# Performance work log

Hardware: AMD Instinct MI355X
Metric: run time of the kernel (lower is better)

## Reference

```python
import jax, jax.numpy as jnp
import numpy as np


def setup_inputs() -> dict:
    key = jax.random.key(0)
    ks = jax.random.split(key, 8)
    N, E = 100000, 3200000
    IN, H, OUT = 256, 128, 64
    x = jax.random.normal(ks[0], (N, IN), dtype=jnp.float32)
    src = jax.random.randint(ks[1], (E,), 0, N, dtype=jnp.int64)
    dst = jax.random.randint(ks[2], (E,), 0, N, dtype=jnp.int64)
    # Glorot-ish scaled weights
    W1_self = jax.random.normal(ks[3], (IN, H), dtype=jnp.float32) / np.sqrt(IN)
    W1_neigh = jax.random.normal(ks[4], (IN, H), dtype=jnp.float32) / np.sqrt(IN)
    b1 = jnp.zeros((H,), dtype=jnp.float32)
    W2_self = jax.random.normal(ks[5], (H, OUT), dtype=jnp.float32) / np.sqrt(H)
    W2_neigh = jax.random.normal(ks[6], (H, OUT), dtype=jnp.float32) / np.sqrt(H)
    b2 = jnp.zeros((OUT,), dtype=jnp.float32)
    return {"x": x, "src": src, "dst": dst,
            "W1_self": W1_self, "W1_neigh": W1_neigh, "b1": b1,
            "W2_self": W2_self, "W2_neigh": W2_neigh, "b2": b2}


def _sage_mean(h, src, dst, W_self, W_neigh, b, deg_inv):
    # mean aggregation over in-neighbors (edges src -> dst)
    N = h.shape[0]
    agg = jax.ops.segment_sum(h[src], dst, num_segments=N)  # [N, F]
    h_neigh = agg * deg_inv[:, None]
    return h @ W_self + h_neigh @ W_neigh + b


def reference(x, src, dst, W1_self, W1_neigh, b1, W2_self, W2_neigh, b2):
    N = x.shape[0]
    deg = jax.ops.segment_sum(jnp.ones_like(dst, dtype=x.dtype), dst, num_segments=N)
    deg_inv = 1.0 / jnp.maximum(deg, 1.0)  # DGL clamps in-degree to >= 1
    h = _sage_mean(x, src, dst, W1_self, W1_neigh, b1, deg_inv)
    h = jax.nn.relu(h)
    h = _sage_mean(h, src, dst, W2_self, W2_neigh, b2, deg_inv)
    return h
```

## Files before the change

### kernel.cpp

```cpp
#include <hip/hip_runtime.h>
#include <hip/hip_bf16.h>


typedef unsigned int uint32;
typedef __attribute__((ext_vector_type(8))) short short8;
typedef __attribute__((ext_vector_type(4))) float f32x4;

#define NBMAX 1024
#define EPB   8192

#if defined(__has_builtin)
#if __has_builtin(__builtin_amdgcn_cvt_pk_f32_fp8) && __has_builtin(__builtin_amdgcn_cvt_pk_fp8_f32)
#define FP8_HW 1
#endif
#endif
#ifndef FP8_HW
#define FP8_HW 0
#endif

__device__ __forceinline__ unsigned short f2bf(float f) {
    unsigned u = __float_as_uint(f);
    u += 0x7fffu + ((u >> 16) & 1u);
    return (unsigned short)(u >> 16);
}
__device__ __forceinline__ uint32 pack2bf(float lo, float hi) {
    return (uint32)f2bf(lo) | ((uint32)f2bf(hi) << 16);
}
__device__ __forceinline__ float bf_lo(uint32 v) { return __uint_as_float(v << 16); }
__device__ __forceinline__ float bf_hi(uint32 v) { return __uint_as_float(v & 0xFFFF0000u); }

__device__ __forceinline__ unsigned char enc8(float v) {
#if FP8_HW
    return (unsigned char)(__builtin_amdgcn_cvt_pk_fp8_f32(v, v, 0, false) & 0xFF);
#else
    float g = v * 0x1p-120f;
    uint32 b = __float_as_uint(g);
    uint32 s = (b >> 24) & 0x80u;
    b &= 0x7fffffffu;
    b += 0x7ffffu + ((b >> 20) & 1u);
    int t = (int)(b >> 20) - 960;
    t = t < 0 ? 0 : (t > 126 ? 126 : t);
    return (unsigned char)(s | (uint32)t);
#endif
}
#if !FP8_HW
__device__ __forceinline__ float dec1(uint32 b) {
    uint32 bits = ((b & 0x80u) << 24) | ((b & 0x7fu) << 20);
    return __uint_as_float(bits) * 0x1p+120f;
}
#endif
__device__ __forceinline__ void dec_u32(uint32 u, float& f0, float& f1, float& f2, float& f3) {
#if FP8_HW
    auto lo = __builtin_amdgcn_cvt_pk_f32_fp8(u, false);
    auto hi = __builtin_amdgcn_cvt_pk_f32_fp8(u, true);
    f0 = lo[0]; f1 = lo[1]; f2 = hi[0]; f3 = hi[1];
#else
    f0 = dec1(u & 0xffu); f1 = dec1((u >> 8) & 0xffu);
    f2 = dec1((u >> 16) & 0xffu); f3 = dec1(u >> 24);
#endif
}

__global__ __launch_bounds__(256) void k_bucket_count(const int* __restrict__ dst, int E,
                                                      int* __restrict__ bcnt) {
    __shared__ int hist[NBMAX];
    for (int i = threadIdx.x; i < NBMAX; i += 256) hist[i] = 0;
    __syncthreads();
    int base = blockIdx.x * EPB;
    #pragma unroll 4
    for (int i = 0; i < EPB / 256; ++i) {
        int e = base + i * 256 + threadIdx.x;
        if (e < E) atomicAdd(&hist[dst[e] >> 7], 1);
    }
    __syncthreads();
    for (int i = threadIdx.x; i < NBMAX; i += 256) {
        int h = hist[i];
        if (h) atomicAdd(&bcnt[i], h);
    }
}

__global__ __launch_bounds__(1024) void k_bucket_scan(const int* __restrict__ bcnt, int NB,
                                                      int* __restrict__ boffs, int* __restrict__ gfill,
                                                      int E) {
    __shared__ int sd[1024];
    int tid = threadIdx.x;
    int v = (tid < NB) ? bcnt[tid] : 0;
    sd[tid] = v;
    __syncthreads();
    for (int off = 1; off < 1024; off <<= 1) {
        int t = (tid >= off) ? sd[tid - off] : 0;
        __syncthreads();
        sd[tid] += t;
        __syncthreads();
    }
    int excl = sd[tid] - v;
    if (tid < NB) { boffs[tid] = excl; gfill[tid] = excl; }
    if (tid == 0) boffs[NB] = E;
}

__global__ __launch_bounds__(256) void k_bucket_scatter(const int* __restrict__ src,
                                                        const int* __restrict__ dst, int E,
                                                        int* __restrict__ gfill,
                                                        uint32* __restrict__ pairs) {
    __shared__ int hist[NBMAX];
    __shared__ int basea[NBMAX];
    for (int i = threadIdx.x; i < NBMAX; i += 256) hist[i] = 0;
    __syncthreads();
    int base = blockIdx.x * EPB;
    #pragma unroll 4
    for (int i = 0; i < EPB / 256; ++i) {
        int e = base + i * 256 + threadIdx.x;
        if (e < E) atomicAdd(&hist[dst[e] >> 7], 1);
    }
    __syncthreads();
    for (int i = threadIdx.x; i < NBMAX; i += 256) {
        int h = hist[i];
        basea[i] = h ? atomicAdd(&gfill[i], h) : 0;
        hist[i] = 0;
    }
    __syncthreads();
    #pragma unroll 4
    for (int i = 0; i < EPB / 256; ++i) {
        int e = base + i * 256 + threadIdx.x;
        if (e < E) {
            int d = dst[e];
            int b = d >> 7;
            int pos = basea[b] + atomicAdd(&hist[b], 1);
            pairs[pos] = ((uint32)src[e] << 7) | (uint32)(d & 127);
        }
    }
}

__global__ __launch_bounds__(256) void k_bucket_sort(const uint32* __restrict__ pairs,
                                                     const int* __restrict__ boffs,
                                                     int N, int E,
                                                     int* __restrict__ row_start,
                                                     float* __restrict__ deg_inv,
                                                     int* __restrict__ src_sorted) {
    __shared__ int cnt[128];
    __shared__ int sc[128];
    __shared__ int fill[128];
    int b = blockIdx.x, tid = threadIdx.x;
    int s0 = boffs[b], s1 = boffs[b + 1];
    if (tid < 128) cnt[tid] = 0;
    __syncthreads();
    for (int e = s0 + tid; e < s1; e += 256)
        atomicAdd(&cnt[pairs[e] & 127], 1);
    __syncthreads();
    if (tid < 128) sc[tid] = cnt[tid];
    __syncthreads();
    for (int off = 1; off < 128; off <<= 1) {
        int v = 0;
        if (tid < 128 && tid >= off) v = sc[tid - off];
        __syncthreads();
        if (tid < 128) sc[tid] += v;
        __syncthreads();
    }
    if (tid < 128) {
        int excl = sc[tid] - cnt[tid];
        int node = b * 128 + tid;
        if (node < N) {
            row_start[node] = s0 + excl;
            int d = cnt[tid];
            deg_inv[node] = 1.0f / (float)(d > 1 ? d : 1);
        }
        fill[tid] = s0 + excl;
    }
    if (b == 0 && tid == 0) row_start[N] = E;
    __syncthreads();
    for (int e = s0 + tid; e < s1; e += 256) {
        uint32 p = pairs[e];
        int pos = atomicAdd(&fill[p & 127], 1);
        src_sorted[pos] = (int)(p >> 7);
    }
}

__global__ __launch_bounds__(256) void k_cast_x(const float* __restrict__ x, uint32* __restrict__ xb,
                                                long n8, long total8) {
    long t = (long)blockIdx.x * blockDim.x + threadIdx.x;
    if (t >= total8) return;
    uint4 o = make_uint4(0u, 0u, 0u, 0u);
    if (t < n8) {
        const float4* p = reinterpret_cast<const float4*>(x) + t * 2;
        float4 a = p[0], b = p[1];
        o.x = pack2bf(a.x, a.y); o.y = pack2bf(a.z, a.w);
        o.z = pack2bf(b.x, b.y); o.w = pack2bf(b.z, b.w);
    }
    reinterpret_cast<uint4*>(xb)[t] = o;
}

__global__ __launch_bounds__(256) void k_wt(const float* __restrict__ Ws, const float* __restrict__ Wn,
                                            int K, int logK, int halfC, unsigned short* __restrict__ Wt) {
    int t = blockIdx.x * blockDim.x + threadIdx.x;
    int total = 2 * halfC * K;
    if (t >= total) return;
    int c = t >> logK, k = t & (K - 1);
    float v = (c < halfC) ? Ws[(size_t)k * halfC + c] : Wn[(size_t)k * halfC + (c - halfC)];
    Wt[t] = f2bf(v);
}

template<int K, int NF, bool YSPLIT>
__global__ __launch_bounds__(512) void gemm_rs(const unsigned short* __restrict__ A, int nstrip,
                                               const unsigned short* __restrict__ Wt,
                                               unsigned short* __restrict__ S16,
                                               unsigned char* __restrict__ N8) {
    constexpr int KS = K / 32;
    __shared__ unsigned short Bs[NF * KS * 512];
    const int tid = threadIdx.x;
    const int wave = tid >> 6, lane = tid & 63;
    const int l15 = lane & 15, l4 = lane >> 4;

    const unsigned short* Wtblk = Wt + (YSPLIT ? (size_t)blockIdx.y * 128 * K : 0);
    const bool out8 = YSPLIT && (blockIdx.y == 1);

    for (int i = tid; i < NF * KS * 64; i += 512) {
        int f = i >> 6, l = i & 63;
        int s = f / NF, n = f - s * NF;
        int col = n * 16 + (l & 15);
        int k = s * 32 + (l >> 4) * 8;
        uint4 v = *reinterpret_cast<const uint4*>(&Wtblk[(size_t)col * K + k]);
        *reinterpret_cast<uint4*>(&Bs[(size_t)i * 8]) = v;
    }
    __syncthreads();

    const unsigned short* Bl = Bs + (size_t)lane * 8;
    const int stride = gridDim.x;
    int g = blockIdx.x;
    if (g >= nstrip) return;

    uint4 uA[KS], uB[KS];

    auto loadA = [&](int gg, uint4* u) {
        int arow = gg * 128 + wave * 16 + l15;
        const unsigned short* Ar = A + (size_t)arow * K + l4 * 8;
        #pragma unroll
        for (int s = 0; s < KS; ++s)
            u[s] = *reinterpret_cast<const uint4*>(Ar + s * 32);
    };

    auto compute = [&](int gc, uint4* u) {
        f32x4 acc[NF] = {};
        #pragma unroll
        for (int s = 0; s < KS; ++s) {
            union { uint4 q; short8 v; } cv;
            cv.q = u[s];
            short8 af = cv.v;
            #pragma unroll
            for (int n = 0; n < NF; ++n) {
                short8 bf = *reinterpret_cast<const short8*>(Bl + (size_t)(s * NF + n) * 512);
                acc[n] = __builtin_amdgcn_mfma_f32_16x16x32_bf16(af, bf, acc[n], 0, 0, 0);
            }
        }
        const int rbase = gc * 128 + wave * 16;
        #pragma unroll
        for (int n = 0; n < NF; ++n) {
            #pragma unroll
            for (int r = 0; r < 4; ++r) {
                int rw = rbase + l4 * 4 + r;
                if constexpr (YSPLIT) {
                    int col = n * 16 + l15;
                    if (out8) N8[(size_t)rw * 128 + col] = enc8(acc[n][r]);
                    else      S16[(size_t)rw * 128 + col] = f2bf(acc[n][r]);
                } else {
                    if (n < 4) S16[(size_t)rw * 64 + n * 16 + l15] = f2bf(acc[n][r]);
                    else       N8[(size_t)rw * 64 + (n - 4) * 16 + l15] = enc8(acc[n][r]);
                }
            }
        }
    };

    loadA(g, uA);
    while (true) {
        int gn = g + stride;
        if (gn < nstrip) loadA(gn, uB);
        compute(g, uA);
        if (gn >= nstrip) break;
        g = gn;
        gn = g + stride;
        if (gn < nstrip) loadA(gn, uA);
        compute(g, uB);
        if (gn >= nstrip) break;
        g = gn;
    }
}

__global__ __launch_bounds__(256) void k_agg1(const uint2* __restrict__ t1n, const uint4* __restrict__ t1s,
                                              const int* __restrict__ rs, const int* __restrict__ ss,
                                              const float* __restrict__ dinv, const float* __restrict__ b1,
                                              uint4* __restrict__ h, int N) {
    int wid  = (blockIdx.x * blockDim.x + threadIdx.x) >> 6;
    int lane = threadIdx.x & 63;
    if (wid >= N) return;
    int e0 = rs[wid], e1 = rs[wid + 1];
    const int q = lane >> 4, c = lane & 15;
    float a0 = 0, a1 = 0, a2 = 0, a3 = 0, a4 = 0, a5 = 0, a6 = 0, a7 = 0;
    float f0, f1, f2, f3;
    int e = e0;
    for (; e + 16 <= e1; e += 16) {
        int s0 = ss[e + q];
        int s1 = ss[e + 4 + q];
        int s2 = ss[e + 8 + q];
        int s3 = ss[e + 12 + q];
        uint2 v0 = t1n[(size_t)s0 * 16 + c];
        uint2 v1 = t1n[(size_t)s1 * 16 + c];
        uint2 v2 = t1n[(size_t)s2 * 16 + c];
        uint2 v3 = t1n[(size_t)s3 * 16 + c];
        dec_u32(v0.x, f0, f1, f2, f3); a0 += f0; a1 += f1; a2 += f2; a3 += f3;
        dec_u32(v0.y, f0, f1, f2, f3); a4 += f0; a5 += f1; a6 += f2; a7 += f3;
        dec_u32(v1.x, f0, f1, f2, f3); a0 += f0; a1 += f1; a2 += f2; a3 += f3;
        dec_u32(v1.y, f0, f1, f2, f3); a4 += f0; a5 += f1; a6 += f2; a7 += f3;
        dec_u32(v2.x, f0, f1, f2, f3); a0 += f0; a1 += f1; a2 += f2; a3 += f3;
        dec_u32(v2.y, f0, f1, f2, f3); a4 += f0; a5 += f1; a6 += f2; a7 += f3;
        dec_u32(v3.x, f0, f1, f2, f3); a0 += f0; a1 += f1; a2 += f2; a3 += f3;
        dec_u32(v3.y, f0, f1, f2, f3); a4 += f0; a5 += f1; a6 += f2; a7 += f3;
    }
    for (; e < e1; e += 4) {
        if (e + q < e1) {
            int s = ss[e + q];
            uint2 v = t1n[(size_t)s * 16 + c];
            dec_u32(v.x, f0, f1, f2, f3); a0 += f0; a1 += f1; a2 += f2; a3 += f3;
            dec_u32(v.y, f0, f1, f2, f3); a4 += f0; a5 += f1; a6 += f2; a7 += f3;
        }
    }
    a0 += __shfl_xor(a0, 16); a1 += __shfl_xor(a1, 16); a2 += __shfl_xor(a2, 16); a3 += __shfl_xor(a3, 16);
    a4 += __shfl_xor(a4, 16); a5 += __shfl_xor(a5, 16); a6 += __shfl_xor(a6, 16); a7 += __shfl_xor(a7, 16);
    a0 += __shfl_xor(a0, 32); a1 += __shfl_xor(a1, 32); a2 += __shfl_xor(a2, 32); a3 += __shfl_xor(a3, 32);
    a4 += __shfl_xor(a4, 32); a5 += __shfl_xor(a5, 32); a6 += __shfl_xor(a6, 32); a7 += __shfl_xor(a7, 32);
    if (lane < 16) {
        float di = dinv[wid];
        uint4 sv = t1s[(size_t)wid * 16 + c];
        float4 bA = *reinterpret_cast<const float4*>(&b1[c * 8]);
        float4 bB = *reinterpret_cast<const float4*>(&b1[c * 8 + 4]);
        float h0 = fmaxf(fmaf(a0, di, bf_lo(sv.x)) + bA.x, 0.f);
        float h1 = fmaxf(fmaf(a1, di, bf_hi(sv.x)) + bA.y, 0.f);
        float h2 = fmaxf(fmaf(a2, di, bf_lo(sv.y)) + bA.z, 0.f);
        float h3 = fmaxf(fmaf(a3, di, bf_hi(sv.y)) + bA.w, 0.f);
        float h4 = fmaxf(fmaf(a4, di, bf_lo(sv.z)) + bB.x, 0.f);
        float h5 = fmaxf(fmaf(a5, di, bf_hi(sv.z)) + bB.y, 0.f);
        float h6 = fmaxf(fmaf(a6, di, bf_lo(sv.w)) + bB.z, 0.f);
        float h7 = fmaxf(fmaf(a7, di, bf_hi(sv.w)) + bB.w, 0.f);
        uint4 o;
        o.x = pack2bf(h0, h1); o.y = pack2bf(h2, h3);
        o.z = pack2bf(h4, h5); o.w = pack2bf(h6, h7);
        h[(size_t)wid * 16 + c] = o;
    }
}

__global__ __launch_bounds__(256) void k_agg2(const uint2* __restrict__ t2n, const uint4* __restrict__ t2s,
                                              const int* __restrict__ rs, const int* __restrict__ ss,
                                              const float* __restrict__ dinv, const float* __restrict__ b2,
                                              float* __restrict__ out, int N) {
    int wid  = (blockIdx.x * blockDim.x + threadIdx.x) >> 6;
    int lane = threadIdx.x & 63;
    if (wid >= N) return;
    int e0 = rs[wid], e1 = rs[wid + 1];
    const int o8 = lane >> 3, c = lane & 7;
    float a0 = 0, a1 = 0, a2 = 0, a3 = 0, a4 = 0, a5 = 0, a6 = 0, a7 = 0;
    float f0, f1, f2, f3;
    int e = e0;
    for (; e + 32 <= e1; e += 32) {
        int s0 = ss[e + o8];
        int s1 = ss[e + 8 + o8];
        int s2 = ss[e + 16 + o8];
        int s3 = ss[e + 24 + o8];
        uint2 v0 = t2n[(size_t)s0 * 8 + c];
        uint2 v1 = t2n[(size_t)s1 * 8 + c];
        uint2 v2 = t2n[(size_t)s2 * 8 + c];
        uint2 v3 = t2n[(size_t)s3 * 8 + c];
        dec_u32(v0.x, f0, f1, f2, f3); a0 += f0; a1 += f1; a2 += f2; a3 += f3;
        dec_u32(v0.y, f0, f1, f2, f3); a4 += f0; a5 += f1; a6 += f2; a7 += f3;
        dec_u32(v1.x, f0, f1, f2, f3); a0 += f0; a1 += f1; a2 += f2; a3 += f3;
        dec_u32(v1.y, f0, f1, f2, f3); a4 += f0; a5 += f1; a6 += f2; a7 += f3;
        dec_u32(v2.x, f0, f1, f2, f3); a0 += f0; a1 += f1; a2 += f2; a3 += f3;
        dec_u32(v2.y, f0, f1, f2, f3); a4 += f0; a5 += f1; a6 += f2; a7 += f3;
        dec_u32(v3.x, f0, f1, f2, f3); a0 += f0; a1 += f1; a2 += f2; a3 += f3;
        dec_u32(v3.y, f0, f1, f2, f3); a4 += f0; a5 += f1; a6 += f2; a7 += f3;
    }
    for (; e < e1; e += 8) {
        if (e + o8 < e1) {
            int s = ss[e + o8];
            uint2 v = t2n[(size_t)s * 8 + c];
            dec_u32(v.x, f0, f1, f2, f3); a0 += f0; a1 += f1; a2 += f2; a3 += f3;
            dec_u32(v.y, f0, f1, f2, f3); a4 += f0; a5 += f1; a6 += f2; a7 += f3;
        }
    }
    a0 += __shfl_xor(a0, 8);  a1 += __shfl_xor(a1, 8);  a2 += __shfl_xor(a2, 8);  a3 += __shfl_xor(a3, 8);
    a4 += __shfl_xor(a4, 8);  a5 += __shfl_xor(a5, 8);  a6 += __shfl_xor(a6, 8);  a7 += __shfl_xor(a7, 8);
    a0 += __shfl_xor(a0, 16); a1 += __shfl_xor(a1, 16); a2 += __shfl_xor(a2, 16); a3 += __shfl_xor(a3, 16);
    a4 += __shfl_xor(a4, 16); a5 += __shfl_xor(a5, 16); a6 += __shfl_xor(a6, 16); a7 += __shfl_xor(a7, 16);
    a0 += __shfl_xor(a0, 32); a1 += __shfl_xor(a1, 32); a2 += __shfl_xor(a2, 32); a3 += __shfl_xor(a3, 32);
    a4 += __shfl_xor(a4, 32); a5 += __shfl_xor(a5, 32); a6 += __shfl_xor(a6, 32); a7 += __shfl_xor(a7, 32);
    if (lane < 8) {
        float di = dinv[wid];
        uint4 sv = t2s[(size_t)wid * 8 + c];
        float4 bA = *reinterpret_cast<const float4*>(&b2[c * 8]);
        float4 bB = *reinterpret_cast<const float4*>(&b2[c * 8 + 4]);
        float4 oA, oB;
        oA.x = fmaf(a0, di, bf_lo(sv.x)) + bA.x;
        oA.y = fmaf(a1, di, bf_hi(sv.x)) + bA.y;
        oA.z = fmaf(a2, di, bf_lo(sv.y)) + bA.z;
        oA.w = fmaf(a3, di, bf_hi(sv.y)) + bA.w;
        oB.x = fmaf(a4, di, bf_lo(sv.z)) + bB.x;
        oB.y = fmaf(a5, di, bf_hi(sv.z)) + bB.y;
        oB.z = fmaf(a6, di, bf_lo(sv.w)) + bB.z;
        oB.w = fmaf(a7, di, bf_hi(sv.w)) + bB.w;
        *reinterpret_cast<float4*>(&out[(size_t)wid * 64 + c * 8]) = oA;
        *reinterpret_cast<float4*>(&out[(size_t)wid * 64 + c * 8 + 4]) = oB;
    }
}

extern "C" void kernel_launch(void* const* d_in, const int* in_sizes, int n_in,
                              void* d_out, int out_size, void* d_ws, size_t ws_size,
                              hipStream_t stream) {
    const float* x   = (const float*)d_in[0];
    const int*   src = (const int*)d_in[1];
    const int*   dst = (const int*)d_in[2];
    const float* W1s = (const float*)d_in[3];
    const float* W1n = (const float*)d_in[4];
    const float* b1  = (const float*)d_in[5];
    const float* W2s = (const float*)d_in[6];
    const float* W2n = (const float*)d_in[7];
    const float* b2  = (const float*)d_in[8];
    float* out = (float*)d_out;

    const int IN = 256, H = 128, OUT = 64;
    const int N  = in_sizes[0] / IN;
    const int E  = in_sizes[1];
    const int Mpad = (N + 127) & ~127;
    const int NB = (N + 127) >> 7;

    char* ws = (char*)d_ws;
    size_t off = 0;
    auto alloc = [&](size_t bytes) -> char* {
        char* p = ws + off;
        off = (off + bytes + 255) & ~(size_t)255;
        return p;
    };
    int*   row_start  = (int*)  alloc((size_t)(N + 1) * 4);
    float* deg_inv    = (float*)alloc((size_t)N * 4);
    int*   bcnt       = (int*)  alloc((size_t)NBMAX * 4);
    int*   boffs      = (int*)  alloc((size_t)(NBMAX + 1) * 4);
    int*   gfill      = (int*)  alloc((size_t)NBMAX * 4);
    int*   src_sorted = (int*)  alloc((size_t)E * 4);
    uint32* pairs     = (uint32*)alloc((size_t)E * 4);
    unsigned short* xb  = (unsigned short*)alloc((size_t)Mpad * IN * 2);
    unsigned short* Wt1 = (unsigned short*)alloc((size_t)(2 * H) * IN * 2);
    unsigned short* Wt2 = (unsigned short*)alloc((size_t)(2 * OUT) * H * 2);
    unsigned short* t1s = (unsigned short*)alloc((size_t)Mpad * H * 2);
    unsigned char*  t1n = (unsigned char*) alloc((size_t)Mpad * H);
    unsigned short* hbf = (unsigned short*)alloc((size_t)Mpad * H * 2);

    hipMemsetAsync(bcnt, 0, (size_t)NBMAX * 4, stream);
    int nblk = (E + EPB - 1) / EPB;
    k_bucket_count  <<<nblk, 256, 0, stream>>>(dst, E, bcnt);
    k_bucket_scan   <<<1, 1024, 0, stream>>>(bcnt, NB, boffs, gfill, E);
    k_bucket_scatter<<<nblk, 256, 0, stream>>>(src, dst, E, gfill, pairs);
    k_bucket_sort   <<<NB, 256, 0, stream>>>(pairs, boffs, N, E, row_start, deg_inv, src_sorted);

    long n8 = (long)N * IN / 8, total8 = (long)Mpad * IN / 8;
    k_cast_x<<<(int)((total8 + 255) / 256), 256, 0, stream>>>(x, (uint32*)xb, n8, total8);
    k_wt<<<(2 * H * IN + 255) / 256, 256, 0, stream>>>(W1s, W1n, IN, 8, H, Wt1);
    k_wt<<<(2 * OUT * H + 255) / 256, 256, 0, stream>>>(W2s, W2n, H, 7, OUT, Wt2);

    int nstrip1 = Mpad / 128;
    gemm_rs<256, 8, true><<<dim3(256, 2), 512, 0, stream>>>(xb, nstrip1, Wt1, t1s, t1n);
    k_agg1<<<(N + 3) / 4, 256, 0, stream>>>((const uint2*)t1n, (const uint4*)t1s,
                                            row_start, src_sorted, deg_inv, b1, (uint4*)hbf, N);
    int nstrip2 = Mpad / 128;
    gemm_rs<128, 8, false><<<dim3(256, 1), 512, 0, stream>>>(hbf, nstrip2, Wt2, t1s, t1n);
    k_agg2<<<(N + 3) / 4, 256, 0, stream>>>((const uint2*)t1n, (const uint4*)t1s,
                                            row_start, src_sorted, deg_inv, b2, out, N);
}
```

Baseline: 322.5 us.

## Split edge bucket scatter into two-level coarse then fine radix passes

Replaces the single scatter of edges into roughly 782 destination buckets with two passes. The first pass scatters into about 25 coarse buckets of 4096 nodes; the second pass regroups each coarse bucket into 32 fine buckets of 128 nodes. Writes go to far fewer open buckets per pass, which should improve write coalescing and reduce shared-atomic contention. The cost is an extra full read and write of the edge pairs array and one more kernel launch. The per-block edge chunk is also halved.

After: 303.8 us. -5.8%, faster.

```diff
diff --git a/kernel.cpp b/kernel.cpp
--- a/kernel.cpp
+++ b/kernel.cpp
@@ -7,7 +7,8 @@
 typedef __attribute__((ext_vector_type(4))) float f32x4;
 
 #define NBMAX 1024
-#define EPB   8192
+#define NQMAX 32
+#define EPB   4096
 
 #if defined(__has_builtin)
 #if __has_builtin(__builtin_amdgcn_cvt_pk_f32_fp8) && __has_builtin(__builtin_amdgcn_cvt_pk_fp8_f32)
@@ -60,8 +61,8 @@
 #endif
 }
 
-__global__ __launch_bounds__(256) void k_bucket_count(const int* __restrict__ dst, int E,
-                                                      int* __restrict__ bcnt) {
+__global__ __launch_bounds__(256) void k_hist_fine(const int* __restrict__ dst, int E,
+                                                   int* __restrict__ bcnt) {
     __shared__ int hist[NBMAX];
     for (int i = threadIdx.x; i < NBMAX; i += 256) hist[i] = 0;
     __syncthreads();
@@ -78,12 +79,12 @@
     }
 }
 
-__global__ __launch_bounds__(1024) void k_bucket_scan(const int* __restrict__ bcnt, int NB,
-                                                      int* __restrict__ boffs, int* __restrict__ gfill,
-                                                      int E) {
+__global__ __launch_bounds__(1024) void k_scan(const int* __restrict__ bcnt, int NBF, int NQ,
+                                               int* __restrict__ boffs, int* __restrict__ gfill_fine,
+                                               int* __restrict__ gfillq, int E) {
     __shared__ int sd[1024];
     int tid = threadIdx.x;
-    int v = (tid < NB) ? bcnt[tid] : 0;
+    int v = (tid < NBF) ? bcnt[tid] : 0;
     sd[tid] = v;
     __syncthreads();
     for (int off = 1; off < 1024; off <<= 1) {
@@ -93,29 +94,34 @@
         __syncthreads();
     }
     int excl = sd[tid] - v;
-    if (tid < NB) { boffs[tid] = excl; gfill[tid] = excl; }
-    if (tid == 0) boffs[NB] = E;
-}
-
-__global__ __launch_bounds__(256) void k_bucket_scatter(const int* __restrict__ src,
+    if (tid < NBF) { boffs[tid] = excl; gfill_fine[tid] = excl; }
+    if (tid == 0) boffs[NBF] = E;
+    __syncthreads();
+    if (tid < NQ) {
+        int f = tid * 32;
+        gfillq[tid] = (f < NBF) ? (sd[f] - ((f < NBF) ? bcnt[f] : 0)) : E;
+    }
+}
+
+__global__ __launch_bounds__(256) void k_scatter_coarse(const int* __restrict__ src,
                                                         const int* __restrict__ dst, int E,
-                                                        int* __restrict__ gfill,
-                                                        uint32* __restrict__ pairs) {
-    __shared__ int hist[NBMAX];
-    __shared__ int basea[NBMAX];
-    for (int i = threadIdx.x; i < NBMAX; i += 256) hist[i] = 0;
+                                                        int* __restrict__ gfillq,
+                                                        uint32* __restrict__ pairs1) {
+    __shared__ int hist[NQMAX];
+    __shared__ int basea[NQMAX];
+    if (threadIdx.x < NQMAX) hist[threadIdx.x] = 0;
     __syncthreads();
     int base = blockIdx.x * EPB;
     #pragma unroll 4
     for (int i = 0; i < EPB / 256; ++i) {
         int e = base + i * 256 + threadIdx.x;
-        if (e < E) atomicAdd(&hist[dst[e] >> 7], 1);
-    }
-    __syncthreads();
-    for (int i = threadIdx.x; i < NBMAX; i += 256) {
-        int h = hist[i];
-        basea[i] = h ? atomicAdd(&gfill[i], h) : 0;
-        hist[i] = 0;
+        if (e < E) atomicAdd(&hist[dst[e] >> 12], 1);
+    }
+    __syncthreads();
+    if (threadIdx.x < NQMAX) {
+        int h = hist[threadIdx.x];
+        basea[threadIdx.x] = h ? atomicAdd(&gfillq[threadIdx.x], h) : 0;
+        hist[threadIdx.x] = 0;
     }
     __syncthreads();
     #pragma unroll 4
@@ -123,10 +129,43 @@
         int e = base + i * 256 + threadIdx.x;
         if (e < E) {
             int d = dst[e];
-            int b = d >> 7;
-            int pos = basea[b] + atomicAdd(&hist[b], 1);
-            pairs[pos] = ((uint32)src[e] << 7) | (uint32)(d & 127);
-        }
+            int q = d >> 12;
+            int pos = basea[q] + atomicAdd(&hist[q], 1);
+            pairs1[pos] = ((uint32)src[e] << 12) | (uint32)(d & 4095);
+        }
+    }
+}
+
+__global__ __launch_bounds__(256) void k_scatter_fine(const uint32* __restrict__ pairs1,
+                                                      const int* __restrict__ boffs,
+                                                      const int* __restrict__ qend,
+                                                      int* __restrict__ gfill_fine,
+                                                      uint32* __restrict__ pairs2, int NC) {
+    __shared__ int hist[32];
+    __shared__ int basea[32];
+    const int q = blockIdx.x;
+    const int s0 = boffs[q * 32];
+    const int s1 = qend[q];
+    for (long cb = (long)s0 + (long)blockIdx.y * EPB; cb < s1; cb += (long)NC * EPB) {
+        int cend = (int)((cb + EPB < s1) ? cb + EPB : s1);
+        if (threadIdx.x < 32) hist[threadIdx.x] = 0;
+        __syncthreads();
+        for (int e = (int)cb + threadIdx.x; e < cend; e += 256)
+            atomicAdd(&hist[(pairs1[e] >> 7) & 31], 1);
+        __syncthreads();
+        if (threadIdx.x < 32) {
+            int h = hist[threadIdx.x];
+            basea[threadIdx.x] = h ? atomicAdd(&gfill_fine[q * 32 + threadIdx.x], h) : 0;
+            hist[threadIdx.x] = 0;
+        }
+        __syncthreads();
+        for (int e = (int)cb + threadIdx.x; e < cend; e += 256) {
+            uint32 p = pairs1[e];
+            int fl = (p >> 7) & 31;
+            int pos = basea[fl] + atomicAdd(&hist[fl], 1);
+            pairs2[pos] = p;
+        }
+        __syncthreads();
     }
 }
 
@@ -170,7 +209,7 @@
     for (int e = s0 + tid; e < s1; e += 256) {
         uint32 p = pairs[e];
         int pos = atomicAdd(&fill[p & 127], 1);
-        src_sorted[pos] = (int)(p >> 7);
+        src_sorted[pos] = (int)(p >> 12);
     }
 }
 
@@ -426,7 +465,8 @@
     const int N  = in_sizes[0] / IN;
     const int E  = in_sizes[1];
     const int Mpad = (N + 127) & ~127;
-    const int NB = (N + 127) >> 7;
+    const int NBF = (N + 127) >> 7;
+    const int NQ  = (N + 4095) >> 12;
 
     char* ws = (char*)d_ws;
     size_t off = 0;
@@ -439,9 +479,11 @@
     float* deg_inv    = (float*)alloc((size_t)N * 4);
     int*   bcnt       = (int*)  alloc((size_t)NBMAX * 4);
     int*   boffs      = (int*)  alloc((size_t)(NBMAX + 1) * 4);
-    int*   gfill      = (int*)  alloc((size_t)NBMAX * 4);
+    int*   gfill_fine = (int*)  alloc((size_t)NBMAX * 4);
+    int*   gfillq     = (int*)  alloc((size_t)NQMAX * 4);
     int*   src_sorted = (int*)  alloc((size_t)E * 4);
-    uint32* pairs     = (uint32*)alloc((size_t)E * 4);
+    uint32* pairs1    = (uint32*)alloc((size_t)E * 4);
+    uint32* pairs2    = (uint32*)alloc((size_t)E * 4);
     unsigned short* xb  = (unsigned short*)alloc((size_t)Mpad * IN * 2);
     unsigned short* Wt1 = (unsigned short*)alloc((size_t)(2 * H) * IN * 2);
     unsigned short* Wt2 = (unsigned short*)alloc((size_t)(2 * OUT) * H * 2);
@@ -451,10 +493,11 @@
 
     hipMemsetAsync(bcnt, 0, (size_t)NBMAX * 4, stream);
     int nblk = (E + EPB - 1) / EPB;
-    k_bucket_count  <<<nblk, 256, 0, stream>>>(dst, E, bcnt);
-    k_bucket_scan   <<<1, 1024, 0, stream>>>(bcnt, NB, boffs, gfill, E);
-    k_bucket_scatter<<<nblk, 256, 0, stream>>>(src, dst, E, gfill, pairs);
-    k_bucket_sort   <<<NB, 256, 0, stream>>>(pairs, boffs, N, E, row_start, deg_inv, src_sorted);
+    k_hist_fine     <<<nblk, 256, 0, stream>>>(dst, E, bcnt);
+    k_scan          <<<1, 1024, 0, stream>>>(bcnt, NBF, NQ, boffs, gfill_fine, gfillq, E);
+    k_scatter_coarse<<<nblk, 256, 0, stream>>>(src, dst, E, gfillq, pairs1);
+    k_scatter_fine  <<<dim3(NQ, 32), 256, 0, stream>>>(pairs1, boffs, gfillq, gfill_fine, pairs2, 32);
+    k_bucket_sort   <<<NBF, 256, 0, stream>>>(pairs2, boffs, N, E, row_start, deg_inv, src_sorted);
 
     long n8 = (long)N * IN / 8, total8 = (long)Mpad * IN / 8;
     k_cast_x<<<(int)((total8 + 255) / 256), 256, 0, stream>>>(x, (uint32*)xb, n8, total8);
```
